# Kernel tuning notes

Measured on AMD Instinct MI355X. Metric: run time of the kernel, lower is better.

The kernel has to match this reference:

```python
import jax, jax.numpy as jnp
import numpy as np

NUM_HEADS = 64
DIM = 128
# Rotation schedule: all (i, j) with i < j in row-major order, matching
# GivensRotationPerHead._create_rotation_indices. R = DIM*(DIM-1)//2 = 8128.
_II, _JJ = np.triu_indices(DIM, k=1)


def setup_inputs() -> dict:
    key = jax.random.key(0)
    thetas = jax.random.normal(key, (NUM_HEADS, _II.shape[0]), dtype=jnp.float32) * 0.01
    return {
        "thetas": thetas,
        "rot_i": jnp.asarray(_II, dtype=jnp.int32),
        "rot_j": jnp.asarray(_JJ, dtype=jnp.int32),
    }


def reference(thetas, rot_i, rot_j):
    # thetas: [H, R]; rot_i, rot_j: [R]
    H, R = thetas.shape
    dim = DIM
    # Precompute all cos/sin once ([R, H, 1]) instead of per-step trig.
    c = jnp.cos(thetas.T)[:, :, None]
    s = jnp.sin(thetas.T)[:, :, None]
    Q0 = jnp.broadcast_to(jnp.eye(dim, dtype=thetas.dtype), (H, dim, dim))

    def body(Q, xs):
        i, j, ci, si = xs
        Qi = Q[:, i, :]  # [H, dim]
        Qj = Q[:, j, :]  # [H, dim]
        Q = Q.at[:, i, :].set(ci * Qi + si * Qj)
        Q = Q.at[:, j, :].set(-si * Qi + ci * Qj)
        return Q, None

    Q, _ = jax.lax.scan(body, Q0, (rot_i, rot_j, c, s))
    return Q
```

## Files before the change

kernel.cpp:

```cpp
#include <hip/hip_runtime.h>

#define DIM 128
#define NHEAD 64
#define NROT 8128
#define NSEG28 28
#define MHEAD28 57344
#define KAC 168
#define CSROWS 64

typedef float f4 __attribute__((ext_vector_type(4)));
typedef short bf8 __attribute__((ext_vector_type(8)));
typedef unsigned short u16;

__device__ const int S_A0[NSEG28] = {0,0,0,8,8,8,16,16,16,24,24,32,32,40,40,
                                     48,48,56,56,64,64,72,80,88,96,104,112,120};
__device__ const int S_J0[NSEG28] = {8,56,104,16,64,112,24,72,120,32,80,40,88,48,96,
                                     56,104,64,112,72,120,80,88,96,104,112,120,128};
__device__ const int S_NJ[NSEG28] = {48,48,24,48,48,16,48,48,8,48,48,48,40,48,32,
                                     48,24,48,16,48,8,48,40,32,24,16,8,0};
__device__ const int S_OFF[NSEG28] = {0,3136,6272,7296,10432,13568,14144,17280,20416,
                                      20672,23808,26944,30080,32384,35520,37120,40256,
                                      41280,44416,44992,48128,48384,51520,53824,55424,
                                      56448,57024,57280};
__device__ const int S_INTRA[NSEG28] = {1,0,0,1,0,0,1,0,0,1,0,1,0,1,0,
                                        1,0,1,0,1,0,1,1,1,1,1,1,1};

__device__ __forceinline__ void sincos_poly(float x, float& sn, float& cn) {
    float x2 = x * x;
    sn = x * fmaf(x2, fmaf(x2, 8.33333333e-3f, -1.66666667e-1f), 1.0f);
    cn = fmaf(x2, fmaf(x2, 4.16666667e-2f, -0.5f), 1.0f);
}

__device__ __forceinline__ u16 f2bf(float v) {
    unsigned b = __float_as_uint(v);
    b += 0x7FFF + ((b >> 16) & 1);
    return (u16)(b >> 16);
}
__device__ __forceinline__ float bf2f(u16 h) {
    return __uint_as_float(((unsigned)h) << 16);
}

struct Row { f4 q0, q1, q2, q3; };

__device__ __forceinline__ void ldrow_u(Row& R, const float* p) {
    const f4* c4 = (const f4*)p;
    R.q0 = c4[0]; R.q1 = c4[1]; R.q2 = c4[2]; R.q3 = c4[3];
}

__device__ __forceinline__ float rowv(const Row& R, float p[8], float v) {
#define ROT2(c, s, T) { float pv = p[T]; float nv = fmaf((c), v, -((s) * pv)); \
                        p[T] = fmaf((s), v, (c) * pv); v = nv; }
    ROT2(R.q0.x, R.q0.y, 0) ROT2(R.q0.z, R.q0.w, 1)
    ROT2(R.q1.x, R.q1.y, 2) ROT2(R.q1.z, R.q1.w, 3)
    ROT2(R.q2.x, R.q2.y, 4) ROT2(R.q2.z, R.q2.w, 5)
    ROT2(R.q3.x, R.q3.y, 6) ROT2(R.q3.z, R.q3.w, 7)
#undef ROT2
    return v;
}

__device__ __forceinline__ void store_bf(u16* oh, u16* ol, int idx, float v, bool act) {
    u16 h = f2bf(v);
    u16 l = f2bf(v - bf2f(h));
    if (act) { oh[idx] = h; ol[idx] = l; }
}

__global__ __launch_bounds__(64, 1)
void chain28(const float* __restrict__ th_all,
             u16* __restrict__ MhW, u16* __restrict__ MlW)
{
    __shared__ __align__(16) float csx[56 + 48 * 16];

    const int lane = threadIdx.x;
    const int head = blockIdx.x & 63;
    const int s    = blockIdx.x >> 6;
    const int a0 = S_A0[s], j0 = S_J0[s], nj = S_NJ[s], n = 8 + nj;
    const bool intra = S_INTRA[s] != 0;
    const float* __restrict__ th = th_all + head * NROT;
    u16* __restrict__ oh = MhW + (size_t)head * MHEAD28 + S_OFF[s];
    u16* __restrict__ ol = MlW + (size_t)head * MHEAD28 + S_OFF[s];
    const bool cact = lane < n;
    const int ne = 8 * nj;
    const int d1 = j0 - a0 - 1;

    float thx[6];
    #pragma unroll
    for (int it = 0; it < 6; ++it) {
        if (it * 64 < ne) {
            int e = lane + it * 64;
            int t = e & 7, jr = e >> 3;
            int i = a0 + t;
            thx[it] = th[((i * (255 - i)) >> 1) + d1 - t + jr];
        }
    }
    float thi = 0.0f;
    if (intra && lane < 28) {
        int t1 = 0, rem = lane;
        while (rem >= 7 - t1) { rem -= 7 - t1; ++t1; }
        int t2 = t1 + 1 + rem;
        int i  = a0 + t1;
        thi = th[((i * (255 - i)) >> 1) + (t2 - t1 - 1)];
    }
    #pragma unroll
    for (int it = 0; it < 6; ++it) {
        if (it * 64 < ne) {
            int e = lane + it * 64;
            float sn, cn; sincos_poly(thx[it], sn, cn);
            csx[56 + 2 * e] = cn; csx[56 + 2 * e + 1] = sn;
        }
    }
    if (intra && lane < 28) {
        float sn, cn; sincos_poly(thi, sn, cn);
        csx[2 * lane] = cn; csx[2 * lane + 1] = sn;
    }
    __syncthreads();

    float p[8];
    #pragma unroll
    for (int t = 0; t < 8; ++t) p[t] = (lane == t) ? 1.0f : 0.0f;

    if (intra) {
        int idx = 0;
        #pragma unroll
        for (int t1 = 0; t1 < 8; ++t1) {
            #pragma unroll
            for (int t2 = t1 + 1; t2 < 8; ++t2) {
                float c = csx[2 * idx], sn = csx[2 * idx + 1];
                float pa = p[t1];
                p[t1] = fmaf(c, pa,    sn * p[t2]);
                p[t2] = fmaf(c, p[t2], -(sn * pa));
                ++idx;
            }
        }
    }

    if (nj > 0) {
        const float* cs = csx + 56;
        const int jv = lane - 8;
        Row A0, A1, B0, B1;
        ldrow_u(A0, cs); ldrow_u(A1, cs + 16);
        #pragma unroll 1
        for (int r = 0; r < nj; r += 4) {
            ldrow_u(B0, cs + 16 * (r + 2)); ldrow_u(B1, cs + 16 * (r + 3));
            float v0 = rowv(A0, p, (r     == jv) ? 1.0f : 0.0f);
            float v1 = rowv(A1, p, (r + 1 == jv) ? 1.0f : 0.0f);
            store_bf(oh, ol, (8 + r)     * n + lane, v0, cact);
            store_bf(oh, ol, (8 + r + 1) * n + lane, v1, cact);
            if (r + 4 < nj) { ldrow_u(A0, cs + 16 * (r + 4));
                              ldrow_u(A1, cs + 16 * (r + 5)); }
            float v2 = rowv(B0, p, (r + 2 == jv) ? 1.0f : 0.0f);
            float v3 = rowv(B1, p, (r + 3 == jv) ? 1.0f : 0.0f);
            store_bf(oh, ol, (8 + r + 2) * n + lane, v2, cact);
            store_bf(oh, ol, (8 + r + 3) * n + lane, v3, cact);
        }
    }

    #pragma unroll
    for (int t = 0; t < 8; ++t)
        store_bf(oh, ol, t * n + lane, p[t], cact);
}

__global__ __launch_bounds__(256, 1)
void compose28(const u16* __restrict__ MhA, const u16* __restrict__ MlA,
               float* __restrict__ out)
{
    __shared__ u16 AhT[16][KAC];
    __shared__ u16 AlT[16][KAC];

    const int tid  = threadIdx.x;
    const int lane = tid & 63;
    const int w    = tid >> 6;
    const int head = blockIdx.x & 63;
    const int sl   = blockIdx.x >> 6;
    const int c0   = sl * 16;
    const u16* __restrict__ Mh = MhA + (size_t)head * MHEAD28;
    const u16* __restrict__ Ml = MlA + (size_t)head * MHEAD28;

    {
        int c = tid & 15, rr = tid >> 4, cg = c0 + c;
        for (int k = DIM + rr; k < KAC; k += 16) { AhT[c][k] = 0; AlT[c][k] = 0; }
        for (int r = rr; r < DIM; r += 16) {
            u16 h, l;
            if (r < 56 && cg < 56) { h = Mh[r * 56 + cg]; l = Ml[r * 56 + cg]; }
            else                   { h = (r == cg) ? (u16)0x3F80 : (u16)0; l = 0; }
            AhT[c][r] = h; AlT[c][r] = l;
        }
    }
    __syncthreads();

    const int fr = lane & 15;
    const int fk = (lane >> 4) * 8;
    const int r4 = (lane >> 4) * 4;
    const int ro = 16 * w;

    #pragma unroll 1
    for (int s = 1; s < NSEG28; ++s) {
        const int a0 = S_A0[s], j0 = S_J0[s], n = 8 + S_NJ[s];
        const int nkt = (n + 31) >> 5;
        const u16* __restrict__ Msh = Mh + S_OFF[s];
        const u16* __restrict__ Msl = Ml + S_OFF[s];
        const bool act = ro < n;
        const int rA  = ro + fr;
        const int rAc = (rA < n) ? rA : (n - 1);

        f4 cA = {0, 0, 0, 0};
        #pragma unroll 1
        for (int kt = 0; kt < nkt; ++kt) {
            const int kk  = kt * 32 + fk;
            const int kkc = (kk <= n - 8) ? kk : (n - 8);
            const int brow = (kk < 8) ? (a0 + kk) : ((kk < n) ? (j0 + kk - 8) : 128);
            bf8 bh = *(const bf8*)&AhT[fr][brow];
            bf8 bl = *(const bf8*)&AlT[fr][brow];
            if (act) {
                bf8 ah = *(const bf8*)&Msh[rAc * n + kkc];
                bf8 al = *(const bf8*)&Msl[rAc * n + kkc];
                cA = __builtin_amdgcn_mfma_f32_16x16x32_bf16(ah, bh, cA, 0, 0, 0);
                cA = __builtin_amdgcn_mfma_f32_16x16x32_bf16(ah, bl, cA, 0, 0, 0);
                cA = __builtin_amdgcn_mfma_f32_16x16x32_bf16(al, bh, cA, 0, 0, 0);
                cA = __builtin_amdgcn_mfma_f32_16x16x32_bf16(al, bl, cA, 0, 0, 0);
            }
        }

        __syncthreads();

        const int rowq = ro + r4;
        if (act && rowq < n) {
            const int rg = (rowq < 8) ? (a0 + rowq) : (j0 + rowq - 8);
            float v0 = cA[0], v1 = cA[1], v2 = cA[2], v3 = cA[3];
            u16 h0 = f2bf(v0), h1 = f2bf(v1), h2 = f2bf(v2), h3 = f2bf(v3);
            u16 l0 = f2bf(v0 - bf2f(h0)), l1 = f2bf(v1 - bf2f(h1));
            u16 l2 = f2bf(v2 - bf2f(h2)), l3 = f2bf(v3 - bf2f(h3));
            ushort4 hv; hv.x = h0; hv.y = h1; hv.z = h2; hv.w = h3;
            ushort4 lv; lv.x = l0; lv.y = l1; lv.z = l2; lv.w = l3;
            *(ushort4*)&AhT[fr][rg] = hv;
            *(ushort4*)&AlT[fr][rg] = lv;
        }
        __syncthreads();
    }

    {
        int c = tid & 15, rr = tid >> 4;
        float* o = out + (size_t)head * (DIM * DIM) + c0;
        for (int r = rr; r < DIM; r += 16)
            o[r * DIM + c] = bf2f(AhT[c][r]) + bf2f(AlT[c][r]);
    }
}

#define QA(r, c) Q[(r)][ (c) ^ ((r) & 31) ]
#define ROTP(c, s, T, v) { float pt = p[T]; p[T] = fmaf((c), pt, (s) * (v)); \
                           (v) = fmaf((c), (v), -((s) * pt)); }
__device__ __forceinline__ void rot8q(const Row& r, float p[8], float& v) {
    ROTP(r.q0.x, r.q0.y, 0, v) ROTP(r.q0.z, r.q0.w, 1, v)
    ROTP(r.q1.x, r.q1.y, 2, v) ROTP(r.q1.z, r.q1.w, 3, v)
    ROTP(r.q2.x, r.q2.y, 4, v) ROTP(r.q2.z, r.q2.w, 5, v)
    ROTP(r.q3.x, r.q3.y, 6, v) ROTP(r.q3.z, r.q3.w, 7, v)
}

__global__ __launch_bounds__(64, 1)
void chain_mono(const float* __restrict__ th_all, float* __restrict__ outp)
{
    __shared__ float Q[DIM][64];
    __shared__ __align__(16) float csx[56 + CSROWS * 16];

    const int lane = threadIdx.x;
    const int head = blockIdx.x & 63;
    const int cb   = blockIdx.x >> 6;
    const int col_glob = cb * 64 + lane;
    const float* __restrict__ th = th_all + head * NROT;

    for (int r = 0; r < DIM; ++r)
        QA(r, lane) = (r == col_glob) ? 1.0f : 0.0f;

    #pragma unroll 1
    for (int g = 0; g < 16; ++g) {
        const int a0  = 8 * g;
        const int ntr = 120 - a0;
        float p[8];
        const int nsub = (ntr > CSROWS) ? 2 : 1;
        #pragma unroll 1
        for (int sub = 0; sub < nsub; ++sub) {
            const int r0 = sub * CSROWS;
            const int nr = (ntr - r0) < CSROWS ? (ntr - r0) : CSROWS;
            const int ne = 8 * nr;
            __syncthreads();
            float thx[8];
            #pragma unroll
            for (int it = 0; it < 8; ++it) {
                if (it * 64 < ne) {
                    int e = lane + it * 64;
                    int t = e & 7, jr = r0 + (e >> 3);
                    int i = a0 + t;
                    thx[it] = th[((i * (255 - i)) >> 1) + jr + 7 - t];
                }
            }
            float thi = 0.0f;
            if (sub == 0 && lane < 28) {
                int t1 = 0, rem = lane;
                while (rem >= 7 - t1) { rem -= 7 - t1; ++t1; }
                int t2 = t1 + 1 + rem;
                int i  = a0 + t1;
                thi = th[((i * (255 - i)) >> 1) + (t2 - t1 - 1)];
            }
            #pragma unroll
            for (int it = 0; it < 8; ++it) {
                if (it * 64 < ne) {
                    int e = lane + it * 64;
                    float sn, cn; sincos_poly(thx[it], sn, cn);
                    csx[56 + 2 * e] = cn; csx[56 + 2 * e + 1] = sn;
                }
            }
            if (sub == 0 && lane < 28) {
                float sn, cn; sincos_poly(thi, sn, cn);
                csx[2 * lane] = cn; csx[2 * lane + 1] = sn;
            }
            __syncthreads();

            if (sub == 0) {
                #pragma unroll
                for (int t = 0; t < 8; ++t) p[t] = QA(a0 + t, lane);
                int idx = 0;
                #pragma unroll
                for (int t1 = 0; t1 < 8; ++t1) {
                    #pragma unroll
                    for (int t2 = t1 + 1; t2 < 8; ++t2) {
                        float c = csx[2 * idx], sn = csx[2 * idx + 1];
                        float pa = p[t1];
                        p[t1] = fmaf(c, pa,    sn * p[t2]);
                        p[t2] = fmaf(c, p[t2], -(sn * pa));
                        ++idx;
                    }
                }
            }
            if (nr > 0) {
                const float* cs = csx + 56;
                const int base = a0 + 8 + r0;
                Row A0, A1, B0, B1;
                float vA0, vA1, vB0, vB1;
                auto ldpair = [&](Row& R, float& v, int r) {
                    ldrow_u(R, cs + 16 * r);
                    v = QA(base + r, lane);
                };
                ldpair(A0, vA0, 0); ldpair(A1, vA1, 1);
                #pragma unroll 1
                for (int r = 0; r < nr; r += 4) {
                    ldpair(B0, vB0, r + 2); ldpair(B1, vB1, r + 3);
                    rot8q(A0, p, vA0); rot8q(A1, p, vA1);
                    QA(base + r, lane)     = vA0;
                    QA(base + r + 1, lane) = vA1;
                    if (r + 4 < nr) { ldpair(A0, vA0, r + 4); ldpair(A1, vA1, r + 5); }
                    rot8q(B0, p, vB0); rot8q(B1, p, vB1);
                    QA(base + r + 2, lane) = vB0;
                    QA(base + r + 3, lane) = vB1;
                }
            }
        }
        #pragma unroll
        for (int t = 0; t < 8; ++t) QA(a0 + t, lane) = p[t];
    }

    __syncthreads();
    float* o = outp + head * (DIM * DIM) + col_glob;
    #pragma unroll 1
    for (int r = 0; r < DIM; ++r) o[r * DIM] = QA(r, lane);
}

extern "C" void kernel_launch(void* const* d_in, const int* in_sizes, int n_in,
                              void* d_out, int out_size, void* d_ws, size_t ws_size,
                              hipStream_t stream) {
    const float* thetas = (const float*)d_in[0];
    float* out = (float*)d_out;
    const size_t need = (size_t)NHEAD * MHEAD28 * 2 * sizeof(u16);

    if (ws_size >= need) {
        u16* MhW = (u16*)d_ws;
        u16* MlW = MhW + (size_t)NHEAD * MHEAD28;
        chain28<<<dim3(NSEG28 * NHEAD), dim3(64), 0, stream>>>(thetas, MhW, MlW);
        compose28<<<dim3(8 * NHEAD), dim3(256), 0, stream>>>(MhW, MlW, out);
    } else {
        chain_mono<<<dim3(2 * NHEAD), dim3(64), 0, stream>>>(thetas, out);
    }
}
```

Measured before the change: 41.63 us.

## Run compose stage as a single barrier-free wave with pipelined global loads

The compose kernel drops from four waves per block to one. That single wave loops over the 16-row output tiles of each segment itself, which removes both __syncthreads per segment and the initial barrier. The B operands are read from LDS once per segment before any in-place writes, and the next row tile's A operands are prefetched from global memory while the current tile's MFMAs run. The cost is that each block now does its row tiles one after another, with less parallelism per CU.

```diff
diff --git a/kernel.cpp b/kernel.cpp
--- a/kernel.cpp
+++ b/kernel.cpp
@@ -159,16 +159,14 @@
         store_bf(oh, ol, t * n + lane, p[t], cact);
 }
 
-__global__ __launch_bounds__(256, 1)
-void compose28(const u16* __restrict__ MhA, const u16* __restrict__ MlA,
-               float* __restrict__ out)
+__global__ __launch_bounds__(64, 1)
+void compose_sw(const u16* __restrict__ MhA, const u16* __restrict__ MlA,
+                float* __restrict__ out)
 {
     __shared__ u16 AhT[16][KAC];
     __shared__ u16 AlT[16][KAC];
 
-    const int tid  = threadIdx.x;
-    const int lane = tid & 63;
-    const int w    = tid >> 6;
+    const int lane = threadIdx.x;
     const int head = blockIdx.x & 63;
     const int sl   = blockIdx.x >> 6;
     const int c0   = sl * 16;
@@ -176,71 +174,92 @@
     const u16* __restrict__ Ml = MlA + (size_t)head * MHEAD28;
 
     {
-        int c = tid & 15, rr = tid >> 4, cg = c0 + c;
-        for (int k = DIM + rr; k < KAC; k += 16) { AhT[c][k] = 0; AlT[c][k] = 0; }
-        for (int r = rr; r < DIM; r += 16) {
+        int c = lane & 15, rr = lane >> 4, cg = c0 + c;
+        for (int k = DIM + rr; k < KAC; k += 4) { AhT[c][k] = 0; AlT[c][k] = 0; }
+        for (int r = rr; r < DIM; r += 4) {
             u16 h, l;
             if (r < 56 && cg < 56) { h = Mh[r * 56 + cg]; l = Ml[r * 56 + cg]; }
             else                   { h = (r == cg) ? (u16)0x3F80 : (u16)0; l = 0; }
             AhT[c][r] = h; AlT[c][r] = l;
         }
     }
-    __syncthreads();
 
     const int fr = lane & 15;
     const int fk = (lane >> 4) * 8;
     const int r4 = (lane >> 4) * 4;
-    const int ro = 16 * w;
 
     #pragma unroll 1
     for (int s = 1; s < NSEG28; ++s) {
         const int a0 = S_A0[s], j0 = S_J0[s], n = 8 + S_NJ[s];
-        const int nkt = (n + 31) >> 5;
         const u16* __restrict__ Msh = Mh + S_OFF[s];
         const u16* __restrict__ Msl = Ml + S_OFF[s];
-        const bool act = ro < n;
-        const int rA  = ro + fr;
-        const int rAc = (rA < n) ? rA : (n - 1);
-
-        f4 cA = {0, 0, 0, 0};
+
+        const int kk0 = fk, kk1 = 32 + fk;
+        const int b0 = (kk0 < 8) ? (a0 + kk0) : ((kk0 < n) ? (j0 + kk0 - 8) : 128);
+        const int b1 = (kk1 < 8) ? (a0 + kk1) : ((kk1 < n) ? (j0 + kk1 - 8) : 128);
+        bf8 bh0 = *(const bf8*)&AhT[fr][b0];
+        bf8 bl0 = *(const bf8*)&AlT[fr][b0];
+        bf8 bh1 = *(const bf8*)&AhT[fr][b1];
+        bf8 bl1 = *(const bf8*)&AlT[fr][b1];
+        const bool two = n > 32;
+        const int kc0 = (kk0 <= n - 8) ? kk0 : (n - 8);
+        const int kc1 = (kk1 <= n - 8) ? kk1 : (n - 8);
+
+        bf8 ahA, alA, ahA1, alA1, ahB, alB, ahB1, alB1;
+        {
+            const int rAc = (fr < n) ? fr : (n - 1);
+            ahA = *(const bf8*)&Msh[(size_t)rAc * n + kc0];
+            alA = *(const bf8*)&Msl[(size_t)rAc * n + kc0];
+            if (two) {
+                ahA1 = *(const bf8*)&Msh[(size_t)rAc * n + kc1];
+                alA1 = *(const bf8*)&Msl[(size_t)rAc * n + kc1];
+            }
+        }
         #pragma unroll 1
-        for (int kt = 0; kt < nkt; ++kt) {
-            const int kk  = kt * 32 + fk;
-            const int kkc = (kk <= n - 8) ? kk : (n - 8);
-            const int brow = (kk < 8) ? (a0 + kk) : ((kk < n) ? (j0 + kk - 8) : 128);
-            bf8 bh = *(const bf8*)&AhT[fr][brow];
-            bf8 bl = *(const bf8*)&AlT[fr][brow];
-            if (act) {
-                bf8 ah = *(const bf8*)&Msh[rAc * n + kkc];
-                bf8 al = *(const bf8*)&Msl[rAc * n + kkc];
-                cA = __builtin_amdgcn_mfma_f32_16x16x32_bf16(ah, bh, cA, 0, 0, 0);
-                cA = __builtin_amdgcn_mfma_f32_16x16x32_bf16(ah, bl, cA, 0, 0, 0);
-                cA = __builtin_amdgcn_mfma_f32_16x16x32_bf16(al, bh, cA, 0, 0, 0);
-                cA = __builtin_amdgcn_mfma_f32_16x16x32_bf16(al, bl, cA, 0, 0, 0);
-            }
-        }
-
-        __syncthreads();
-
-        const int rowq = ro + r4;
-        if (act && rowq < n) {
-            const int rg = (rowq < 8) ? (a0 + rowq) : (j0 + rowq - 8);
-            float v0 = cA[0], v1 = cA[1], v2 = cA[2], v3 = cA[3];
-            u16 h0 = f2bf(v0), h1 = f2bf(v1), h2 = f2bf(v2), h3 = f2bf(v3);
-            u16 l0 = f2bf(v0 - bf2f(h0)), l1 = f2bf(v1 - bf2f(h1));
-            u16 l2 = f2bf(v2 - bf2f(h2)), l3 = f2bf(v3 - bf2f(h3));
-            ushort4 hv; hv.x = h0; hv.y = h1; hv.z = h2; hv.w = h3;
-            ushort4 lv; lv.x = l0; lv.y = l1; lv.z = l2; lv.w = l3;
-            *(ushort4*)&AhT[fr][rg] = hv;
-            *(ushort4*)&AlT[fr][rg] = lv;
-        }
-        __syncthreads();
+        for (int ro = 0; ro < n; ro += 16) {
+            const bool have = (ro + 16) < n;
+            if (have) {
+                const int rN  = ro + 16 + fr;
+                const int rNc = (rN < n) ? rN : (n - 1);
+                ahB = *(const bf8*)&Msh[(size_t)rNc * n + kc0];
+                alB = *(const bf8*)&Msl[(size_t)rNc * n + kc0];
+                if (two) {
+                    ahB1 = *(const bf8*)&Msh[(size_t)rNc * n + kc1];
+                    alB1 = *(const bf8*)&Msl[(size_t)rNc * n + kc1];
+                }
+            }
+            f4 acc = {0, 0, 0, 0};
+            acc = __builtin_amdgcn_mfma_f32_16x16x32_bf16(ahA, bh0, acc, 0, 0, 0);
+            acc = __builtin_amdgcn_mfma_f32_16x16x32_bf16(ahA, bl0, acc, 0, 0, 0);
+            acc = __builtin_amdgcn_mfma_f32_16x16x32_bf16(alA, bh0, acc, 0, 0, 0);
+            acc = __builtin_amdgcn_mfma_f32_16x16x32_bf16(alA, bl0, acc, 0, 0, 0);
+            if (two) {
+                acc = __builtin_amdgcn_mfma_f32_16x16x32_bf16(ahA1, bh1, acc, 0, 0, 0);
+                acc = __builtin_amdgcn_mfma_f32_16x16x32_bf16(ahA1, bl1, acc, 0, 0, 0);
+                acc = __builtin_amdgcn_mfma_f32_16x16x32_bf16(alA1, bh1, acc, 0, 0, 0);
+                acc = __builtin_amdgcn_mfma_f32_16x16x32_bf16(alA1, bl1, acc, 0, 0, 0);
+            }
+
+            const int rowq = ro + r4;
+            if (rowq < n) {
+                const int rg = (rowq < 8) ? (a0 + rowq) : (j0 + rowq - 8);
+                float v0 = acc[0], v1 = acc[1], v2 = acc[2], v3 = acc[3];
+                u16 h0 = f2bf(v0), h1 = f2bf(v1), h2 = f2bf(v2), h3 = f2bf(v3);
+                u16 l0 = f2bf(v0 - bf2f(h0)), l1 = f2bf(v1 - bf2f(h1));
+                u16 l2 = f2bf(v2 - bf2f(h2)), l3 = f2bf(v3 - bf2f(h3));
+                ushort4 hv; hv.x = h0; hv.y = h1; hv.z = h2; hv.w = h3;
+                ushort4 lv; lv.x = l0; lv.y = l1; lv.z = l2; lv.w = l3;
+                *(ushort4*)&AhT[fr][rg] = hv;
+                *(ushort4*)&AlT[fr][rg] = lv;
+            }
+            ahA = ahB; alA = alB; ahA1 = ahB1; alA1 = alB1;
+        }
     }
 
     {
-        int c = tid & 15, rr = tid >> 4;
+        int c = lane & 15, rr = lane >> 4;
         float* o = out + (size_t)head * (DIM * DIM) + c0;
-        for (int r = rr; r < DIM; r += 16)
+        for (int r = rr; r < DIM; r += 4)
             o[r * DIM + c] = bf2f(AhT[c][r]) + bf2f(AlT[c][r]);
     }
 }
@@ -374,7 +393,7 @@
         u16* MhW = (u16*)d_ws;
         u16* MlW = MhW + (size_t)NHEAD * MHEAD28;
         chain28<<<dim3(NSEG28 * NHEAD), dim3(64), 0, stream>>>(thetas, MhW, MlW);
-        compose28<<<dim3(8 * NHEAD), dim3(256), 0, stream>>>(MhW, MlW, out);
+        compose_sw<<<dim3(8 * NHEAD), dim3(64), 0, stream>>>(MhW, MlW, out);
     } else {
         chain_mono<<<dim3(2 * NHEAD), dim3(64), 0, stream>>>(thetas, out);
     }
```

Result: slower. 54.64 us (+31.2%).
